# Optimization experiments

Hardware: AMD Instinct MI355X
Metric: run time of the kernel (lower is better)

## Reference

```python
import jax, jax.numpy as jnp
import numpy as np

FFT_LEN = 256
WIN_LEN = 768
FRM_LEN = 128
PPF_TAP = WIN_LEN // FFT_LEN  # 6
SCALE = -256.0
GROUP_DELAY = 648  # module uses group_delay = -648
B, C, S, T = 8, 2, FFT_LEN // 2 + 1, 4096


def _make_lpf(win_len):
    # firwin(win_len, 0.5, window='hann', scale=False) equivalent
    n = np.arange(win_len, dtype=np.float64)
    w = 0.5 - 0.5 * np.cos(2.0 * np.pi * n / (win_len - 1))
    h = w * np.sinc(0.5 * (n - (win_len - 1) / 2.0))
    return jnp.asarray(h, dtype=jnp.float32)


def setup_inputs() -> dict:
    key = jax.random.key(0)
    k1, k2 = jax.random.split(key)
    spectrum_real = jax.random.normal(k1, (B, C, S, T), dtype=jnp.float32)
    spectrum_imag = jax.random.normal(k2, (B, C, S, T), dtype=jnp.float32)
    lpf_coef = _make_lpf(WIN_LEN)
    return {"spectrum_real": spectrum_real, "spectrum_imag": spectrum_imag, "lpf_coef": lpf_coef}


def reference(spectrum_real, spectrum_imag, lpf_coef):
    # spectrum: (B, C, S, T) complex; per-frame irfft over subbands
    spec = jnp.swapaxes(spectrum_real + 1j * spectrum_imag, -1, -2)  # (B,C,T,S)
    fftout = jnp.fft.irfft(spec, n=FFT_LEN, axis=-1)                 # (B,C,T,FFT_LEN)
    rev = fftout[..., ::-1]                                          # comp_in[fft_len-j-1]
    v = jnp.tile(rev, (1, 1, 1, PPF_TAP)) * lpf_coef                 # (B,C,T,WIN_LEN)
    b, c, t, _ = v.shape
    num_samples = t * FRM_LEN
    # overlap-add: frame t contributes v[t] at offset t*FRM_LEN (shifting buffer recurrence)
    idx = jnp.arange(t)[:, None] * FRM_LEN + jnp.arange(WIN_LEN)[None, :]  # (T, WIN_LEN)
    y = jnp.zeros((b, c, num_samples + WIN_LEN), dtype=v.dtype)
    y = y.at[..., idx].add(v)[..., :num_samples]
    y = y * (FRM_LEN * SCALE)
    # circular shift by group delay, then trim the wrapped tail
    y = jnp.roll(y, -GROUP_DELAY, axis=-1)[..., :-GROUP_DELAY]
    return y
```

## Files before the change

### kernel.cpp

```cpp
#include <hip/hip_runtime.h>
#include <hip/hip_bf16.h>
#include <math.h>

#define NBINS   129
#define NFFT    256
#define WINL    768
#define TFRAMES 4096
#define OUTL    523640
#define NQUADS  (OUTL / 4)
#define SHIFT   648
#define WSEG    26
#define CHUNK   (WSEG * 128)
#define NCHUNK  ((OUTL + CHUNK - 1) / CHUNK)
#define FF      32
#define FFS     32

#define KDIM    288
#define KROW    296
#define GROWL   264
#define GROW    268
#define WBYTES  (16 * 9 * 64 * 16)
#define GBYTES  ((size_t)16 * TFRAMES * 256 * 2)
#define NSTG    17
#define NF4     5

typedef __attribute__((ext_vector_type(8))) short bf16x8;
typedef __attribute__((ext_vector_type(4))) float f32x4;

static __device__ __forceinline__ ushort f2bf(float x) {
    union { float f; unsigned u; } v; v.f = x;
    unsigned r = v.u + 0x7FFFu + ((v.u >> 16) & 1u);
    return (ushort)(r >> 16);
}
static __device__ __forceinline__ float bf2f(ushort u) {
    union { unsigned u_; float f; } g; g.u_ = ((unsigned)u) << 16; return g.f;
}

__global__ void build_w_kernel(ushort* __restrict__ wp)
{
    const int gid  = blockIdx.x * 256 + threadIdx.x;
    const int lane = gid & 63;
    const int mtks = gid >> 6;
    const int ks   = mtks % 9;
    const int mt   = mtks / 9;
    const int m    = mt * 16 + (lane & 15);
    const int kb   = ks * 32 + ((lane >> 4) << 3);

    ushort o[8];
    #pragma unroll
    for (int e = 0; e < 8; ++e) {
        const int kap = kb + e;
        float val = 0.f;
        if (kap < 258) {
            const int k = kap >> 1;
            float s, c;
            sincospif((float)(k * (m + 1)) * (1.0f / 128.0f), &s, &c);
            if (kap & 1)  val = (k >= 1 && k <= 127) ? s * (2.0f / 256.0f) : 0.f;
            else          val = (k == 0 || k == 128) ? c * (1.0f / 256.0f)
                                                     : c * (2.0f / 256.0f);
        }
        o[e] = f2bf(val);
    }
    int4 pk;
    pk.x = o[0] | (o[1] << 16); pk.y = o[2] | (o[3] << 16);
    pk.z = o[4] | (o[5] << 16); pk.w = o[6] | (o[7] << 16);
    ((int4*)wp)[gid] = pk;
}

__global__ __launch_bounds__(256, 6)
void pfb_dft_kernel(const float* __restrict__ gre, const float* __restrict__ gim,
                    const ushort* __restrict__ wp, ushort* __restrict__ Gg)
{
    __shared__ ushort s_mem[FF * KROW];
    ushort* s_Bu = s_mem;
    ushort (*s_G)[GROWL] = (ushort (*)[GROWL])s_mem;

    const int t0  = blockIdx.x * FF;
    const int bc  = blockIdx.y;
    const int tid = threadIdx.x;
    const size_t specBase = (size_t)bc * NBINS * TFRAMES;

    const float4* gre4 = (const float4*)(gre + specBase);
    const float4* gim4 = (const float4*)(gim + specBase);
    float4 vr4[NF4], vi4[NF4];
    #pragma unroll
    for (int r = 0; r < NF4; ++r) {
        const int idx4 = tid + r * 256;
        float4 a = {0.f, 0.f, 0.f, 0.f}, b = {0.f, 0.f, 0.f, 0.f};
        if (idx4 < NBINS * (FF / 4)) {
            const int k = idx4 >> 3, f4 = idx4 & 7;
            const size_t o4 = (size_t)k * (TFRAMES / 4) + (size_t)(t0 >> 2) + f4;
            a = gre4[o4]; b = gim4[o4];
        }
        vr4[r] = a; vi4[r] = b;
    }
    #pragma unroll
    for (int r = 0; r < NF4; ++r) {
        const int idx4 = tid + r * 256;
        if (idx4 < NBINS * (FF / 4)) {
            const int k = idx4 >> 3, f4 = idx4 & 7;
            const float rr[4] = {vr4[r].x, vr4[r].y, vr4[r].z, vr4[r].w};
            const float ii[4] = {vi4[r].x, vi4[r].y, vi4[r].z, vi4[r].w};
            #pragma unroll
            for (int j = 0; j < 4; ++j) {
                __hip_bfloat162 p = __float22bfloat162_rn(make_float2(rr[j], ii[j]));
                *(__hip_bfloat162*)&s_Bu[(4 * f4 + j) * KROW + 2 * k] = p;
            }
        }
    }
    for (int idx = tid; idx < FF * (KROW - 258); idx += 256) {
        const int f = idx / (KROW - 258), r2 = idx - f * (KROW - 258);
        s_Bu[f * KROW + 258 + r2] = 0;
    }
    __syncthreads();

    const int lane = tid & 63;
    const int wid  = tid >> 6;
    const int brow = lane & 15;
    const int kq   = lane >> 4;

    f32x4 acc[4][2];
    #pragma unroll
    for (int mi = 0; mi < 4; ++mi)
        #pragma unroll
        for (int nt = 0; nt < 2; ++nt)
            acc[mi][nt] = (f32x4){0.f, 0.f, 0.f, 0.f};

    const ushort* wbase0 = wp + ((size_t)(wid * 4) * 9 * 64 + (size_t)lane) * 8;
    #pragma unroll
    for (int ks = 0; ks < 9; ++ks) {
        const bf16x8 b0 = *(const bf16x8*)&s_Bu[brow * KROW + ks * 32 + (kq << 3)];
        const bf16x8 b1 = *(const bf16x8*)&s_Bu[(16 + brow) * KROW + ks * 32 + (kq << 3)];
        #pragma unroll
        for (int mi = 0; mi < 4; ++mi) {
            const bf16x8 aw = *(const bf16x8*)(wbase0 + mi * 4608 + ks * 512);
            acc[mi][0] = __builtin_amdgcn_mfma_f32_16x16x32_bf16(aw, b0, acc[mi][0], 0, 0, 0);
            acc[mi][1] = __builtin_amdgcn_mfma_f32_16x16x32_bf16(aw, b1, acc[mi][1], 0, 0, 0);
        }
    }
    __syncthreads();

    #pragma unroll
    for (int mi = 0; mi < 4; ++mi) {
        const int m0 = (wid * 4 + mi) * 16 + (kq << 2);
        #pragma unroll
        for (int nt = 0; nt < 2; ++nt) {
            const int f = nt * 16 + brow;
            __hip_bfloat162 lo = __float22bfloat162_rn(make_float2(acc[mi][nt].x, acc[mi][nt].y));
            __hip_bfloat162 hi = __float22bfloat162_rn(make_float2(acc[mi][nt].z, acc[mi][nt].w));
            uint2 pk; pk.x = *(unsigned*)&lo; pk.y = *(unsigned*)&hi;
            *(uint2*)&s_G[f][m0] = pk;
        }
    }
    __syncthreads();

    ushort* gout = Gg + ((size_t)bc * TFRAMES + t0) * NFFT;
    #pragma unroll
    for (int it = 0; it < 4; ++it) {
        const int c = tid + it * 256;
        const int row = c >> 5, chunk = c & 31;
        *(bf16x8*)&gout[c * 8] = *(const bf16x8*)&s_G[row][chunk * 8];
    }
}

__global__ __launch_bounds__(256, 8)
void pfb_oa_kernel(const ushort* __restrict__ Gg, const float* __restrict__ glpf,
                   float* __restrict__ out)
{
    const int tid = threadIdx.x;
    const int bc  = blockIdx.y;
    const int h0  = blockIdx.x * 512 + tid;

    const int b = (4 * h0 + SHIFT) & 127;
    float4 lw[6];
    #pragma unroll
    for (int p = 0; p < 6; ++p) lw[p] = *(const float4*)&glpf[(p << 7) + b];

    const ushort* Gb = Gg + (size_t)bc * TFRAMES * NFFT;
    const size_t outBase = (size_t)bc * OUTL;

    #pragma unroll
    for (int j = 0; j < 2; ++j) {
        const int h = h0 + j * 256;
        int a = (4 * h + SHIFT) >> 7;
        if (a > TFRAMES - 1) a = TFRAMES - 1;
        float s0 = 0.f, s1 = 0.f, s2 = 0.f, s3 = 0.f;
        #pragma unroll
        for (int p = 0; p < 6; ++p) {
            const ushort4 q = *(const ushort4*)&Gb[(size_t)(a - p) * NFFT + b + ((p & 1) << 7)];
            s0 += lw[p].x * bf2f(q.x);
            s1 += lw[p].y * bf2f(q.y);
            s2 += lw[p].z * bf2f(q.z);
            s3 += lw[p].w * bf2f(q.w);
        }
        if (h < NQUADS) {
            float4 o;
            o.x = s0 * (-32768.0f); o.y = s1 * (-32768.0f);
            o.z = s2 * (-32768.0f); o.w = s3 * (-32768.0f);
            *(float4*)&out[outBase + 4 * h] = o;
        }
    }
}

__global__ __launch_bounds__(256, 4)
void pfb_mfma_kernel(const float* __restrict__ gre, const float* __restrict__ gim,
                     const float* __restrict__ glpf, const ushort* __restrict__ wp,
                     float* __restrict__ out)
{
    __shared__ ushort s_bufu[FFS * KROW];
    __shared__ float  s_lpf[WINL];
    ushort* s_Bu = s_bufu;
    ushort (*s_G)[GROW] = (ushort (*)[GROW])s_bufu;

    const int q   = blockIdx.x;
    const int bc  = blockIdx.y;
    const int tid = threadIdx.x;
    const int t0  = WSEG * q;
    const size_t specBase = (size_t)bc * NBINS * TFRAMES;

    for (int idx = tid; idx < WINL; idx += 256) s_lpf[idx] = glpf[idx];

    float vr[NSTG], vi[NSTG];
    #pragma unroll
    for (int r = 0; r < NSTG; ++r) {
        const int idx = tid + r * 256;
        const int k = idx >> 5, f = idx & 31;
        const int t = t0 + f;
        const bool ok = (idx < NBINS * FFS) && (t < TFRAMES);
        float a = 0.f, bb = 0.f;
        if (ok) {
            const size_t g = specBase + (size_t)k * TFRAMES + (size_t)t;
            a = gre[g]; bb = gim[g];
        }
        vr[r] = a; vi[r] = bb;
    }
    #pragma unroll
    for (int r = 0; r < NSTG; ++r) {
        const int idx = tid + r * 256;
        if (idx < NBINS * FFS) {
            const int k = idx >> 5, f = idx & 31;
            __hip_bfloat162 p = __float22bfloat162_rn(make_float2(vr[r], vi[r]));
            *(__hip_bfloat162*)&s_Bu[f * KROW + 2 * k] = p;
        }
    }
    for (int idx = tid; idx < FFS * (KROW - 258); idx += 256) {
        const int f = idx / (KROW - 258), r = idx - f * (KROW - 258);
        s_Bu[f * KROW + 258 + r] = 0;
    }
    __syncthreads();

    const int lane = tid & 63;
    const int wid  = tid >> 6;
    const int brow = lane & 15;
    const int kgrp = (lane >> 4) << 3;

    bf16x8 bfrag[2][9];
    #pragma unroll
    for (int nt = 0; nt < 2; ++nt)
        #pragma unroll
        for (int ks = 0; ks < 9; ++ks)
            bfrag[nt][ks] = *(const bf16x8*)&s_Bu[(nt * 16 + brow) * KROW + ks * 32 + kgrp];

    f32x4 acc[4][2];
    #pragma unroll
    for (int mi = 0; mi < 4; ++mi)
        #pragma unroll
        for (int nt = 0; nt < 2; ++nt)
            acc[mi][nt] = (f32x4){0.f, 0.f, 0.f, 0.f};

    #pragma unroll 1
    for (int mi = 0; mi < 4; ++mi) {
        const ushort* wbase = wp + ((size_t)((wid * 4 + mi) * 9) * 64 + lane) * 8;
        #pragma unroll
        for (int ks = 0; ks < 9; ++ks) {
            const bf16x8 aw = *(const bf16x8*)(wbase + ks * 512);
            acc[mi][0] = __builtin_amdgcn_mfma_f32_16x16x32_bf16(aw, bfrag[0][ks], acc[mi][0], 0, 0, 0);
            acc[mi][1] = __builtin_amdgcn_mfma_f32_16x16x32_bf16(aw, bfrag[1][ks], acc[mi][1], 0, 0, 0);
        }
    }
    __syncthreads();

    #pragma unroll
    for (int mi = 0; mi < 4; ++mi) {
        const int m0 = (wid * 4 + mi) * 16 + ((lane >> 4) << 2);
        #pragma unroll
        for (int nt = 0; nt < 2; ++nt) {
            const int f = nt * 16 + brow;
            __hip_bfloat162 lo = __float22bfloat162_rn(make_float2(acc[mi][nt].x, acc[mi][nt].y));
            __hip_bfloat162 hi = __float22bfloat162_rn(make_float2(acc[mi][nt].z, acc[mi][nt].w));
            uint2 pk; pk.x = *(unsigned*)&lo; pk.y = *(unsigned*)&hi;
            *(uint2*)&s_G[f][m0] = pk;
        }
    }
    __syncthreads();

    const size_t outBase = (size_t)bc * OUTL;
    const int i0 = q * CHUNK;
    #pragma unroll 1
    for (int r = 0; r < 13; ++r) {
        const int i = i0 + r * 256 + tid;
        const int s = i + SHIFT;
        const int tlo = (s - 640) >> 7;
        int thi = s >> 7;
        if (thi > t0 + FFS - 1) thi = t0 + FFS - 1;
        if (thi > TFRAMES - 1) thi = TFRAMES - 1;
        float sum = 0.f;
        #pragma unroll
        for (int u = 0; u < 6; ++u) {
            const int t  = tlo + u;
            int jj = s - (t << 7);
            if (jj < 0) jj = 0;
            const float w = s_lpf[jj];
            sum += (t <= thi) ? w * bf2f(s_G[t - t0][jj & 255]) : 0.f;
        }
        if (i < OUTL) out[outBase + i] = sum * (-32768.0f);
    }
}

extern "C" void kernel_launch(void* const* d_in, const int* in_sizes, int n_in,
                              void* d_out, int out_size, void* d_ws, size_t ws_size,
                              hipStream_t stream)
{
    const float* gre  = (const float*)d_in[0];
    const float* gim  = (const float*)d_in[1];
    const float* glpf = (const float*)d_in[2];
    float* out = (float*)d_out;

    if (ws_size >= (size_t)WBYTES + GBYTES) {
        ushort* wp = (ushort*)d_ws;
        ushort* Gg = (ushort*)((char*)d_ws + WBYTES);
        build_w_kernel<<<36, 256, 0, stream>>>(wp);
        dim3 gridA(TFRAMES / FF, 16);
        pfb_dft_kernel<<<gridA, 256, 0, stream>>>(gre, gim, wp, Gg);
        dim3 gridB((NQUADS + 511) / 512, 16);
        pfb_oa_kernel<<<gridB, 256, 0, stream>>>(Gg, glpf, out);
    } else if (ws_size >= (size_t)WBYTES) {
        ushort* wp = (ushort*)d_ws;
        build_w_kernel<<<36, 256, 0, stream>>>(wp);
        dim3 grid(NCHUNK, 16);
        pfb_mfma_kernel<<<grid, 256, 0, stream>>>(gre, gim, glpf, wp, out);
    }
}
```

Baseline: 52.57 us.

## Warp-specialize DFT kernel into producer/consumer waves with double-buffered LDS

Replaces the single-tile DFT kernel with a 512-thread block in which four producer waves load and convert spectrum tiles into a double-buffered LDS area while four consumer waves run the MFMA DFT on the previous tile. Each block now handles four 32-frame tiles, and results are written straight from registers to global memory instead of being staged through LDS. The aim is to overlap global loads with matrix compute and drop the staging pass. In exchange the grid is four times smaller, so fewer blocks are in flight, and the direct stores write only 8 bytes per thread and are less coalesced.

Result: slower. 71.48 us (+36.0%).

```diff
diff --git a/kernel.cpp b/kernel.cpp
--- a/kernel.cpp
+++ b/kernel.cpp
@@ -13,11 +13,11 @@
 #define CHUNK   (WSEG * 128)
 #define NCHUNK  ((OUTL + CHUNK - 1) / CHUNK)
 #define FF      32
+#define TPB     4
 #define FFS     32
 
 #define KDIM    288
 #define KROW    296
-#define GROWL   264
 #define GROW    268
 #define WBYTES  (16 * 9 * 64 * 16)
 #define GBYTES  ((size_t)16 * TFRAMES * 256 * 2)
@@ -67,99 +67,110 @@
     ((int4*)wp)[gid] = pk;
 }
 
-__global__ __launch_bounds__(256, 6)
-void pfb_dft_kernel(const float* __restrict__ gre, const float* __restrict__ gim,
-                    const ushort* __restrict__ wp, ushort* __restrict__ Gg)
-{
-    __shared__ ushort s_mem[FF * KROW];
-    ushort* s_Bu = s_mem;
-    ushort (*s_G)[GROWL] = (ushort (*)[GROWL])s_mem;
-
-    const int t0  = blockIdx.x * FF;
-    const int bc  = blockIdx.y;
-    const int tid = threadIdx.x;
+__global__ __launch_bounds__(512, 4)
+void pfb_dft_pc_kernel(const float* __restrict__ gre, const float* __restrict__ gim,
+                       const ushort* __restrict__ wp, ushort* __restrict__ Gg)
+{
+    __shared__ ushort s_B[2][FF * KROW];
+
+    const int tid  = threadIdx.x;
+    const int wave = tid >> 6;
+    const int bc   = blockIdx.y;
+    const int tbase = blockIdx.x * (TPB * FF);
     const size_t specBase = (size_t)bc * NBINS * TFRAMES;
-
     const float4* gre4 = (const float4*)(gre + specBase);
     const float4* gim4 = (const float4*)(gim + specBase);
+
+    const bool producer = (wave >= 4);
+    const int  ptid = tid - 256;
+
     float4 vr4[NF4], vi4[NF4];
-    #pragma unroll
-    for (int r = 0; r < NF4; ++r) {
-        const int idx4 = tid + r * 256;
-        float4 a = {0.f, 0.f, 0.f, 0.f}, b = {0.f, 0.f, 0.f, 0.f};
-        if (idx4 < NBINS * (FF / 4)) {
-            const int k = idx4 >> 3, f4 = idx4 & 7;
-            const size_t o4 = (size_t)k * (TFRAMES / 4) + (size_t)(t0 >> 2) + f4;
-            a = gre4[o4]; b = gim4[o4];
-        }
-        vr4[r] = a; vi4[r] = b;
-    }
-    #pragma unroll
-    for (int r = 0; r < NF4; ++r) {
-        const int idx4 = tid + r * 256;
-        if (idx4 < NBINS * (FF / 4)) {
-            const int k = idx4 >> 3, f4 = idx4 & 7;
-            const float rr[4] = {vr4[r].x, vr4[r].y, vr4[r].z, vr4[r].w};
-            const float ii[4] = {vi4[r].x, vi4[r].y, vi4[r].z, vi4[r].w};
-            #pragma unroll
-            for (int j = 0; j < 4; ++j) {
-                __hip_bfloat162 p = __float22bfloat162_rn(make_float2(rr[j], ii[j]));
-                *(__hip_bfloat162*)&s_Bu[(4 * f4 + j) * KROW + 2 * k] = p;
+
+    auto LOAD = [&](int tile) {
+        const int tt0 = tbase + tile * FF;
+        #pragma unroll
+        for (int r = 0; r < NF4; ++r) {
+            const int idx4 = ptid + r * 256;
+            float4 a = {0.f, 0.f, 0.f, 0.f}, b = {0.f, 0.f, 0.f, 0.f};
+            if (idx4 < NBINS * (FF / 4)) {
+                const int k = idx4 >> 3, f4 = idx4 & 7;
+                const size_t o4 = (size_t)k * (TFRAMES / 4) + (size_t)(tt0 >> 2) + f4;
+                a = gre4[o4]; b = gim4[o4];
             }
-        }
-    }
-    for (int idx = tid; idx < FF * (KROW - 258); idx += 256) {
-        const int f = idx / (KROW - 258), r2 = idx - f * (KROW - 258);
-        s_Bu[f * KROW + 258 + r2] = 0;
-    }
+            vr4[r] = a; vi4[r] = b;
+        }
+    };
+    auto WLDS = [&](int buf) {
+        #pragma unroll
+        for (int r = 0; r < NF4; ++r) {
+            const int idx4 = ptid + r * 256;
+            if (idx4 < NBINS * (FF / 4)) {
+                const int k = idx4 >> 3, f4 = idx4 & 7;
+                const float rr[4] = {vr4[r].x, vr4[r].y, vr4[r].z, vr4[r].w};
+                const float ii[4] = {vi4[r].x, vi4[r].y, vi4[r].z, vi4[r].w};
+                #pragma unroll
+                for (int j = 0; j < 4; ++j) {
+                    __hip_bfloat162 p = __float22bfloat162_rn(make_float2(rr[j], ii[j]));
+                    *(__hip_bfloat162*)&s_B[buf][(4 * f4 + j) * KROW + 2 * k] = p;
+                }
+            }
+        }
+    };
+
+    for (int idx = tid; idx < 2 * FF * (KROW - 258); idx += 512) {
+        const int bu  = idx / (FF * (KROW - 258));
+        const int rem = idx - bu * (FF * (KROW - 258));
+        const int f = rem / (KROW - 258), r2 = rem - f * (KROW - 258);
+        s_B[bu][f * KROW + 258 + r2] = 0;
+    }
+    if (producer) { LOAD(0); WLDS(0); }
     __syncthreads();
 
     const int lane = tid & 63;
-    const int wid  = tid >> 6;
     const int brow = lane & 15;
     const int kq   = lane >> 4;
-
-    f32x4 acc[4][2];
-    #pragma unroll
-    for (int mi = 0; mi < 4; ++mi)
-        #pragma unroll
-        for (int nt = 0; nt < 2; ++nt)
-            acc[mi][nt] = (f32x4){0.f, 0.f, 0.f, 0.f};
-
-    const ushort* wbase0 = wp + ((size_t)(wid * 4) * 9 * 64 + (size_t)lane) * 8;
-    #pragma unroll
-    for (int ks = 0; ks < 9; ++ks) {
-        const bf16x8 b0 = *(const bf16x8*)&s_Bu[brow * KROW + ks * 32 + (kq << 3)];
-        const bf16x8 b1 = *(const bf16x8*)&s_Bu[(16 + brow) * KROW + ks * 32 + (kq << 3)];
-        #pragma unroll
-        for (int mi = 0; mi < 4; ++mi) {
-            const bf16x8 aw = *(const bf16x8*)(wbase0 + mi * 4608 + ks * 512);
-            acc[mi][0] = __builtin_amdgcn_mfma_f32_16x16x32_bf16(aw, b0, acc[mi][0], 0, 0, 0);
-            acc[mi][1] = __builtin_amdgcn_mfma_f32_16x16x32_bf16(aw, b1, acc[mi][1], 0, 0, 0);
-        }
-    }
-    __syncthreads();
-
-    #pragma unroll
-    for (int mi = 0; mi < 4; ++mi) {
-        const int m0 = (wid * 4 + mi) * 16 + (kq << 2);
-        #pragma unroll
-        for (int nt = 0; nt < 2; ++nt) {
-            const int f = nt * 16 + brow;
-            __hip_bfloat162 lo = __float22bfloat162_rn(make_float2(acc[mi][nt].x, acc[mi][nt].y));
-            __hip_bfloat162 hi = __float22bfloat162_rn(make_float2(acc[mi][nt].z, acc[mi][nt].w));
-            uint2 pk; pk.x = *(unsigned*)&lo; pk.y = *(unsigned*)&hi;
-            *(uint2*)&s_G[f][m0] = pk;
-        }
-    }
-    __syncthreads();
-
-    ushort* gout = Gg + ((size_t)bc * TFRAMES + t0) * NFFT;
-    #pragma unroll
-    for (int it = 0; it < 4; ++it) {
-        const int c = tid + it * 256;
-        const int row = c >> 5, chunk = c & 31;
-        *(bf16x8*)&gout[c * 8] = *(const bf16x8*)&s_G[row][chunk * 8];
+    const ushort* wbase0 = wp + ((size_t)(wave * 4) * 9 * 64 + (size_t)lane) * 8;
+
+    #pragma unroll 1
+    for (int i = 0; i < TPB; ++i) {
+        if (producer) {
+            if (i + 1 < TPB) { LOAD(i + 1); WLDS((i + 1) & 1); }
+        } else {
+            const ushort* sB = s_B[i & 1];
+            f32x4 acc[4][2];
+            #pragma unroll
+            for (int mi = 0; mi < 4; ++mi)
+                #pragma unroll
+                for (int nt = 0; nt < 2; ++nt)
+                    acc[mi][nt] = (f32x4){0.f, 0.f, 0.f, 0.f};
+
+            #pragma unroll
+            for (int ks = 0; ks < 9; ++ks) {
+                const bf16x8 b0 = *(const bf16x8*)&sB[brow * KROW + ks * 32 + (kq << 3)];
+                const bf16x8 b1 = *(const bf16x8*)&sB[(16 + brow) * KROW + ks * 32 + (kq << 3)];
+                #pragma unroll
+                for (int mi = 0; mi < 4; ++mi) {
+                    const bf16x8 aw = *(const bf16x8*)(wbase0 + mi * 4608 + ks * 512);
+                    acc[mi][0] = __builtin_amdgcn_mfma_f32_16x16x32_bf16(aw, b0, acc[mi][0], 0, 0, 0);
+                    acc[mi][1] = __builtin_amdgcn_mfma_f32_16x16x32_bf16(aw, b1, acc[mi][1], 0, 0, 0);
+                }
+            }
+
+            ushort* gout = Gg + ((size_t)bc * TFRAMES + tbase + i * FF) * NFFT;
+            #pragma unroll
+            for (int mi = 0; mi < 4; ++mi) {
+                const int m0 = (wave * 4 + mi) * 16 + (kq << 2);
+                #pragma unroll
+                for (int nt = 0; nt < 2; ++nt) {
+                    const int f = nt * 16 + brow;
+                    __hip_bfloat162 lo = __float22bfloat162_rn(make_float2(acc[mi][nt].x, acc[mi][nt].y));
+                    __hip_bfloat162 hi = __float22bfloat162_rn(make_float2(acc[mi][nt].z, acc[mi][nt].w));
+                    uint2 pk; pk.x = *(unsigned*)&lo; pk.y = *(unsigned*)&hi;
+                    *(uint2*)&gout[f * NFFT + m0] = pk;
+                }
+            }
+        }
+        __syncthreads();
     }
 }
 
@@ -330,8 +341,8 @@
         ushort* wp = (ushort*)d_ws;
         ushort* Gg = (ushort*)((char*)d_ws + WBYTES);
         build_w_kernel<<<36, 256, 0, stream>>>(wp);
-        dim3 gridA(TFRAMES / FF, 16);
-        pfb_dft_kernel<<<gridA, 256, 0, stream>>>(gre, gim, wp, Gg);
+        dim3 gridA(TFRAMES / (TPB * FF), 16);
+        pfb_dft_pc_kernel<<<gridA, 512, 0, stream>>>(gre, gim, wp, Gg);
         dim3 gridB((NQUADS + 511) / 512, 16);
         pfb_oa_kernel<<<gridB, 256, 0, stream>>>(Gg, glpf, out);
     } else if (ws_size >= (size_t)WBYTES) {
```
